# Kernel optimization log

Hardware: AMD Instinct MI355X
Metric: run time of the kernel (lower is better)

The kernel has to match this reference:

```python
import jax, jax.numpy as jnp
import numpy as np

N_SRC = 100000

def setup_inputs() -> dict:
    key = jax.random.key(0)
    k1, k2, k3 = jax.random.split(key, 3)
    feat_src = jax.random.normal(k1, (N_SRC, 64), dtype=jnp.float32)
    edge_src = jax.random.randint(k2, (1250000,), 0, N_SRC, dtype=jnp.int64)
    edge_dst = jax.random.randint(k3, (1250000,), 0, 50000, dtype=jnp.int64)
    return {"feat_src": feat_src, "edge_src": edge_src, "edge_dst": edge_dst, "n_dst": 50000}

def reference(feat_src, edge_src, edge_dst, n_dst):
    n_src = feat_src.shape[0]
    ones = jnp.ones(edge_src.shape[0], dtype=feat_src.dtype)
    # out-degree of src nodes, in-degree of dst nodes
    deg_out = jax.ops.segment_sum(ones, edge_src, num_segments=n_src)
    deg_in = jax.ops.segment_sum(ones, edge_dst, num_segments=n_dst)
    norm_src = jax.lax.rsqrt(jnp.clip(deg_out, 1.0))  # [n_src]
    norm_dst = jax.lax.rsqrt(jnp.clip(deg_in, 1.0))   # [n_dst]
    # gather -> scale -> scatter-sum
    msg = feat_src[edge_src] * norm_src[edge_src][:, None]      # [E, d]
    rst = jax.ops.segment_sum(msg, edge_dst, num_segments=n_dst)  # [n_dst, d]
    return rst * norm_dst[:, None]
```

## Files before the change

### kernel.cpp

```cpp
#include <hip/hip_runtime.h>

#define NFEAT 64
#define SCAN_BLOCKS 128

#define NB_IN  128
#define NB_OUT 64
#define LWORDS 12512

__global__ __launch_bounds__(1024) void v28_hist(
        const int* __restrict__ esrc, const int* __restrict__ edst,
        unsigned char* __restrict__ cnt_in, unsigned char* __restrict__ cnt_out,
        int E, int n_src, int n_dst, int Ec_in, int Ec_out, int srange) {
    __shared__ unsigned int lh[LWORDS];
    int blk = blockIdx.x, t = threadIdx.x, T = blockDim.x;
    const int* idx; unsigned char* row; int rbase, W, lo, hi;
    if (blk < NB_IN) {
        idx = edst; rbase = 0; W = n_dst;
        row = cnt_in + (size_t)blk * n_dst;
        lo = blk * Ec_in; hi = lo + Ec_in;
    } else {
        int p    = (blk - NB_IN) / NB_OUT;
        int brel = (blk - NB_IN) % NB_OUT;
        idx = esrc; rbase = p * srange;
        W = n_src - rbase; if (W > srange) W = srange;
        row = cnt_out + (size_t)brel * n_src + rbase;
        lo = brel * Ec_out; hi = lo + Ec_out;
    }
    if (hi > E) hi = E;
    if (W <= 0) return;
    int Wp = (W + 3) >> 2;
    for (int i = t; i < Wp; i += T) lh[i] = 0;
    __syncthreads();
    if (lo < hi) {
        int nq = (hi - lo) >> 2;
#define V28_H(val)                                                            \
        {                                                                     \
            unsigned r = (unsigned)((val) - rbase);                           \
            if (r < (unsigned)W)                                              \
                atomicAdd(&lh[r >> 2], 1u << ((r & 3) << 3));                 \
        }
        for (int q = t; q < nq; q += T) {
            int i = lo + (q << 2);
            int4 e = *(const int4*)(idx + i);
            V28_H(e.x) V28_H(e.y) V28_H(e.z) V28_H(e.w)
        }
        for (int i = lo + (nq << 2) + t; i < hi; i += T) V28_H(idx[i]);
#undef V28_H
    }
    __syncthreads();
    if ((((uintptr_t)row) & 3) == 0 && (W & 3) == 0) {
        unsigned int* row32 = (unsigned int*)row;
        for (int i = t; i < Wp; i += T) row32[i] = lh[i];
    } else {
        for (int i = t; i < W; i += T)
            row[i] = (unsigned char)((lh[i >> 2] >> ((i & 3) << 3)) & 0xff);
    }
}

__global__ void v28_normscan(const unsigned char* __restrict__ cnt_out,
                             unsigned char* __restrict__ cnt_in,
                             int* __restrict__ deg_in,
                             float* __restrict__ nsrc, float* __restrict__ ndst,
                             int* __restrict__ bsum, int n_src, int n_dst) {
    __shared__ int red[256];
    int b = blockIdx.x, t = threadIdx.x;
    int cs = (n_src + SCAN_BLOCKS - 1) / SCAN_BLOCKS;
    int slo = b * cs, shi = slo + cs; if (shi > n_src) shi = n_src;
    for (int i = slo + t; i < shi; i += 256) {
        const unsigned char* p = cnt_out + i;
        int s = 0;
        for (int j = 0; j < NB_OUT; ++j) { s += *p; p += n_src; }
        nsrc[i] = rsqrtf(fmaxf((float)s, 1.0f));
    }
    int cd = (n_dst + SCAN_BLOCKS - 1) / SCAN_BLOCKS;
    int dlo = b * cd, dhi = dlo + cd; if (dhi > n_dst) dhi = n_dst;
    int tot = 0;
    for (int i = dlo + t; i < dhi; i += 256) {
        unsigned char* p = cnt_in + i;
        int a = 0;
        for (int j = 0; j < NB_IN; ++j) {
            int c = *p;
            *p = (unsigned char)a;
            a += c;
            p += n_dst;
        }
        deg_in[i] = a;
        ndst[i] = rsqrtf(fmaxf((float)a, 1.0f));
        tot += a;
    }
    red[t] = tot;
    __syncthreads();
    for (int o = 128; o > 0; o >>= 1) {
        if (t < o) red[t] += red[t + o];
        __syncthreads();
    }
    if (t == 0) bsum[b] = red[0];
}

__global__ void v28_rowstart(const int* __restrict__ deg_in,
                             const int* __restrict__ bsum,
                             int* __restrict__ row_start, int n_dst) {
    __shared__ int tsum[256];
    __shared__ int boffs;
    int b = blockIdx.x, t = threadIdx.x;
    int cd = (n_dst + SCAN_BLOCKS - 1) / SCAN_BLOCKS;
    int lo = b * cd, hi = lo + cd; if (hi > n_dst) hi = n_dst;
    if (t == 0) {
        int a = 0;
        for (int k = 0; k < b; ++k) a += bsum[k];
        boffs = a;
    }
    int per = (cd + 255) / 256;
    int mylo = lo + t * per;
    int myhi = mylo + per; if (myhi > hi) myhi = hi;
    int s = 0;
    for (int i = mylo; i < myhi; ++i) s += deg_in[i];
    tsum[t] = s;
    __syncthreads();
    if (t == 0) {
        int a = 0;
        for (int k = 0; k < 256; ++k) { int v = tsum[k]; tsum[k] = a; a += v; }
    }
    __syncthreads();
    int a = boffs + tsum[t];
    for (int i = mylo; i < myhi; ++i) { row_start[i] = a; a += deg_in[i]; }
    if (b == SCAN_BLOCKS - 1 && t == 255) row_start[n_dst] = a;
}

__global__ __launch_bounds__(1024) void v28_place(
        const int* __restrict__ esrc, const int* __restrict__ edst,
        const unsigned char* __restrict__ pre, const int* __restrict__ row_start,
        int* __restrict__ sorted_src, int E, int n_dst, int Ec) {
    __shared__ unsigned int lh[LWORDS];
    int b = blockIdx.x, t = threadIdx.x, T = blockDim.x;
    int Wp = (n_dst + 3) >> 2;
    for (int i = t; i < Wp; i += T) lh[i] = 0;
    __syncthreads();
    int lo = b * Ec;
    int hi = lo + Ec; if (hi > E) hi = E;
    if (lo >= hi) return;
    const unsigned char* prow = pre + (size_t)b * n_dst;
    int nq = (hi - lo) >> 2;
#define V28_PL(dd, ss)                                                       \
    {                                                                        \
        unsigned r = (unsigned)(dd);                                         \
        if (r < (unsigned)n_dst) {                                           \
            int sh = (r & 3) << 3;                                           \
            unsigned old = atomicAdd(&lh[r >> 2], 1u << sh);                 \
            int rank = (old >> sh) & 0xff;                                   \
            int slot = row_start[r] + (int)prow[r] + rank;                   \
            if ((unsigned)slot < (unsigned)E) sorted_src[slot] = (ss);       \
        }                                                                    \
    }
    for (int q = t; q < nq; q += T) {
        int i = lo + (q << 2);
        int4 dv = *(const int4*)(edst + i);
        int4 sv = *(const int4*)(esrc + i);
        V28_PL(dv.x, sv.x)
        V28_PL(dv.y, sv.y)
        V28_PL(dv.z, sv.z)
        V28_PL(dv.w, sv.w)
    }
    for (int i = lo + (nq << 2) + t; i < hi; i += T) {
        int d = edst[i];
        int s = esrc[i];
        V28_PL(d, s)
    }
#undef V28_PL
}

__global__ void v26_gather(const float* __restrict__ feat,
                           const int* __restrict__ sorted_src,
                           const int* __restrict__ row_start,
                           const float* __restrict__ nsrc,
                           const float* __restrict__ ndst,
                           float* __restrict__ out,
                           int n_src, int n_dst) {
    int gid = blockIdx.x * blockDim.x + threadIdx.x;
    int d = gid >> 6;
    if (d >= n_dst) return;
    int lane = threadIdx.x & 63;
    int g = lane >> 4;
    int lg = lane & 15;
    int lo = row_start[d], hi = row_start[d + 1];
    int nmax = n_src - 1;
    float4 a0 = {0,0,0,0}, a1 = {0,0,0,0}, a2 = {0,0,0,0}, a3 = {0,0,0,0};
#define V26_G(kk, acc)                                                        \
    {                                                                         \
        int s_ = sorted_src[(kk) + g];                                        \
        s_ = min(max(s_, 0), nmax);                                           \
        float w_ = nsrc[s_];                                                  \
        float4 v_ = *(const float4*)(feat + (size_t)s_ * NFEAT + (lg << 2));  \
        acc.x += v_.x * w_; acc.y += v_.y * w_;                               \
        acc.z += v_.z * w_; acc.w += v_.w * w_;                               \
    }
    int k = lo;
    for (; k + 15 < hi; k += 16) {
        V26_G(k, a0)
        V26_G(k + 4, a1)
        V26_G(k + 8, a2)
        V26_G(k + 12, a3)
    }
    for (; k + 3 < hi; k += 4) {
        V26_G(k, a0)
    }
    if (k + g < hi) {
        V26_G(k, a1)
    }
#undef V26_G
    float4 a;
    a.x = (a0.x + a1.x) + (a2.x + a3.x);
    a.y = (a0.y + a1.y) + (a2.y + a3.y);
    a.z = (a0.z + a1.z) + (a2.z + a3.z);
    a.w = (a0.w + a1.w) + (a2.w + a3.w);
    a.x += __shfl_xor(a.x, 16); a.x += __shfl_xor(a.x, 32);
    a.y += __shfl_xor(a.y, 16); a.y += __shfl_xor(a.y, 32);
    a.z += __shfl_xor(a.z, 16); a.z += __shfl_xor(a.z, 32);
    a.w += __shfl_xor(a.w, 16); a.w += __shfl_xor(a.w, 32);
    if (g == 0) {
        float sc = ndst[d];
        float4 r;
        r.x = a.x * sc; r.y = a.y * sc; r.z = a.z * sc; r.w = a.w * sc;
        *(float4*)(out + (size_t)d * NFEAT + (lg << 2)) = r;
    }
}


__global__ void v23_zero(int* __restrict__ deg_out, int* __restrict__ deg_in,
                         int n_src, int n_dst) {
    int i = blockIdx.x * blockDim.x + threadIdx.x;
    if (i < n_src) deg_out[i] = 0;
    if (i < n_dst) deg_in[i] = 0;
}

__global__ void v23_deg(const int* __restrict__ esrc, const int* __restrict__ edst,
                        int* __restrict__ deg_out, int* __restrict__ deg_in,
                        int E, int n_src, int n_dst) {
    int i = blockIdx.x * blockDim.x + threadIdx.x;
    if (i >= E) return;
    int s = esrc[i];
    int d = edst[i];
    if ((unsigned)s < (unsigned)n_src) atomicAdd(&deg_out[s], 1);
    if ((unsigned)d < (unsigned)n_dst) atomicAdd(&deg_in[d], 1);
}

__global__ void v23_norm(const int* __restrict__ deg_out, const int* __restrict__ deg_in,
                         float* __restrict__ nsrc, float* __restrict__ ndst,
                         int n_src, int n_dst) {
    int i = blockIdx.x * blockDim.x + threadIdx.x;
    if (i < n_src) nsrc[i] = rsqrtf(fmaxf((float)deg_out[i], 1.0f));
    if (i < n_dst) ndst[i] = rsqrtf(fmaxf((float)deg_in[i], 1.0f));
}

__global__ void v23_scan1(const int* __restrict__ deg_in, int* __restrict__ bsum,
                          int n_dst, int chunk) {
    __shared__ int red[256];
    int b = blockIdx.x, t = threadIdx.x;
    int lo = b * chunk;
    int hi = lo + chunk; if (hi > n_dst) hi = n_dst;
    int s = 0;
    for (int i = lo + t; i < hi; i += 256) s += deg_in[i];
    red[t] = s;
    __syncthreads();
    for (int o = 128; o > 0; o >>= 1) {
        if (t < o) red[t] += red[t + o];
        __syncthreads();
    }
    if (t == 0) bsum[b] = red[0];
}

__global__ void v23_scan2(int* __restrict__ bsum, int* __restrict__ boff,
                          int* __restrict__ row_start, int n_dst) {
    if (threadIdx.x == 0) {
        int a = 0;
        for (int k = 0; k < SCAN_BLOCKS; ++k) { boff[k] = a; a += bsum[k]; }
        row_start[n_dst] = a;
    }
}

__global__ void v23_scan3(const int* __restrict__ deg_in, const int* __restrict__ boff,
                          int* __restrict__ row_start, int* __restrict__ cursor,
                          int n_dst, int chunk) {
    __shared__ int tsum[256];
    int b = blockIdx.x, t = threadIdx.x;
    int lo = b * chunk;
    int hi = lo + chunk; if (hi > n_dst) hi = n_dst;
    int per = (chunk + 255) / 256;
    int mylo = lo + t * per;
    int myhi = mylo + per; if (myhi > hi) myhi = hi;
    int s = 0;
    for (int i = mylo; i < myhi; ++i) s += deg_in[i];
    tsum[t] = s;
    __syncthreads();
    if (t == 0) {
        int a = 0;
        for (int k = 0; k < 256; ++k) { int v = tsum[k]; tsum[k] = a; a += v; }
    }
    __syncthreads();
    int a = boff[b] + tsum[t];
    for (int i = mylo; i < myhi; ++i) {
        row_start[i] = a;
        cursor[i] = a;
        a += deg_in[i];
    }
}

__global__ void v23_place(const int* __restrict__ esrc, const int* __restrict__ edst,
                          int* __restrict__ cursor, int* __restrict__ sorted_src,
                          int E, int n_src, int n_dst) {
    int i = blockIdx.x * blockDim.x + threadIdx.x;
    if (i >= E) return;
    int s = esrc[i];
    int d = edst[i];
    if ((unsigned)s >= (unsigned)n_src) return;
    if ((unsigned)d >= (unsigned)n_dst) return;
    int slot = atomicAdd(&cursor[d], 1);
    sorted_src[slot] = s;
}


extern "C" void kernel_launch(void* const* d_in, const int* in_sizes, int n_in,
                              void* d_out, int out_size, void* d_ws, size_t ws_size,
                              hipStream_t stream) {
    const float* feat = (const float*)d_in[0];
    const int* esrc = (const int*)d_in[1];
    const int* edst = (const int*)d_in[2];
    float* out = (float*)d_out;

    const int n_src = in_sizes[0] / NFEAT;
    const int E     = in_sizes[1];
    const int n_dst = out_size / NFEAT;

    const int B = 256;
    int nmax = n_src > n_dst ? n_src : n_dst;
    int chunk = (n_dst + SCAN_BLOCKS - 1) / SCAN_BLOCKS;

    int srange = (((n_src + 1) / 2) + 3) & ~3;

    size_t sz_cnt_in  = ((size_t)NB_IN  * (size_t)n_dst + 255) & ~(size_t)255;
    size_t sz_cnt_out = ((size_t)NB_OUT * (size_t)n_src + 255) & ~(size_t)255;
    size_t sz_fixed = (size_t)E * 4
                    + (size_t)n_dst * 4
                    + (size_t)n_src * 4
                    + (size_t)n_dst * 4
                    + (size_t)(n_dst + 1) * 4
                    + (size_t)n_dst * 4
                    + (size_t)SCAN_BLOCKS * 8 + 512;
    bool big = (ws_size >= sz_cnt_in + sz_cnt_out + sz_fixed)
             && (n_dst <= LWORDS * 4) && (srange <= LWORDS * 4);

    if (big) {
        char* ws = (char*)d_ws;
        size_t off = 0;
        unsigned char* cnt_in  = (unsigned char*)(ws + off); off += sz_cnt_in;
        unsigned char* cnt_out = (unsigned char*)(ws + off); off += sz_cnt_out;
        int*   sorted_src = (int*)(ws + off);   off += (size_t)E * 4;
        int*   deg_in     = (int*)(ws + off);   off += (size_t)n_dst * 4;
        float* nsrc       = (float*)(ws + off); off += (size_t)n_src * 4;
        float* ndst       = (float*)(ws + off); off += (size_t)n_dst * 4;
        int*   row_start  = (int*)(ws + off);   off += (size_t)(n_dst + 1) * 4;
        int*   bsum       = (int*)(ws + off);   off += SCAN_BLOCKS * 4;

        int Ec_in  = (((E + NB_IN  - 1) / NB_IN ) + 3) & ~3;
        int Ec_out = (((E + NB_OUT - 1) / NB_OUT) + 3) & ~3;

        v28_hist<<<NB_IN + 2 * NB_OUT, 1024, 0, stream>>>(
            esrc, edst, cnt_in, cnt_out, E, n_src, n_dst, Ec_in, Ec_out, srange);
        v28_normscan<<<SCAN_BLOCKS, B, 0, stream>>>(
            cnt_out, cnt_in, deg_in, nsrc, ndst, bsum, n_src, n_dst);
        v28_rowstart<<<SCAN_BLOCKS, B, 0, stream>>>(deg_in, bsum, row_start, n_dst);
        v28_place<<<NB_IN, 1024, 0, stream>>>(esrc, edst, cnt_in, row_start,
                                              sorted_src, E, n_dst, Ec_in);
        long long gthreads = (long long)n_dst * 64;
        v26_gather<<<(int)((gthreads + B - 1) / B), B, 0, stream>>>(feat, sorted_src,
                                                                    row_start, nsrc, ndst,
                                                                    out, n_src, n_dst);
    } else {
        char* ws = (char*)d_ws;
        size_t off = 0;
        int*   deg_out    = (int*)(ws + off);   off += (size_t)n_src * 4;
        int*   deg_in     = (int*)(ws + off);   off += (size_t)n_dst * 4;
        float* nsrc       = (float*)(ws + off); off += (size_t)n_src * 4;
        float* ndst       = (float*)(ws + off); off += (size_t)n_dst * 4;
        int*   row_start  = (int*)(ws + off);   off += (size_t)(n_dst + 1) * 4;
        int*   cursor     = (int*)(ws + off);   off += (size_t)n_dst * 4;
        int*   bsum       = (int*)(ws + off);   off += SCAN_BLOCKS * 4;
        int*   boff       = (int*)(ws + off);   off += SCAN_BLOCKS * 4;
        int*   sorted_src = (int*)(ws + off);   off += (size_t)E * 4;

        v23_zero<<<(nmax + B - 1) / B, B, 0, stream>>>(deg_out, deg_in, n_src, n_dst);
        v23_deg<<<(E + B - 1) / B, B, 0, stream>>>(esrc, edst, deg_out, deg_in,
                                                   E, n_src, n_dst);
        v23_norm<<<(nmax + B - 1) / B, B, 0, stream>>>(deg_out, deg_in, nsrc, ndst,
                                                       n_src, n_dst);
        v23_scan1<<<SCAN_BLOCKS, B, 0, stream>>>(deg_in, bsum, n_dst, chunk);
        v23_scan2<<<1, 64, 0, stream>>>(bsum, boff, row_start, n_dst);
        v23_scan3<<<SCAN_BLOCKS, B, 0, stream>>>(deg_in, boff, row_start, cursor,
                                                 n_dst, chunk);
        v23_place<<<(E + B - 1) / B, B, 0, stream>>>(esrc, edst, cursor, sorted_src,
                                                     E, n_src, n_dst);
        long long gthreads = (long long)n_dst * 64;
        v26_gather<<<(int)((gthreads + B - 1) / B), B, 0, stream>>>(feat, sorted_src,
                                                                    row_start, nsrc, ndst,
                                                                    out, n_src, n_dst);
    }
}
```

Measured before the change: 205.4 us.

## Restructure CSR build: 2D-tiled histograms, per-node norm/scan, preloaded place offsets

The fused histogram kernel is split into two launches on 2D grids. Each range tile is sized to fit shared memory, and the block counts rise (256 in, 128 out). The normalisation and scan now run one thread per node, with a single-pass exclusive scan in place of the serial rowstart loop. The place kernel preloads each block's prefix bytes into shared memory so the atomic returns the full rank directly, removing a global byte read per edge. This adds more partial-count rows to reduce and more launches. The fast path now also requires node counts divisible by four and at most 65536 dst nodes.

```diff
diff --git a/kernel.cpp b/kernel.cpp
--- a/kernel.cpp
+++ b/kernel.cpp
@@ -1,39 +1,29 @@
 #include <hip/hip_runtime.h>
 
 #define NFEAT 64
-#define SCAN_BLOCKS 128
-
-#define NB_IN  128
-#define NB_OUT 64
-#define LWORDS 12512
-
-__global__ __launch_bounds__(1024) void v28_hist(
-        const int* __restrict__ esrc, const int* __restrict__ edst,
-        unsigned char* __restrict__ cnt_in, unsigned char* __restrict__ cnt_out,
-        int E, int n_src, int n_dst, int Ec_in, int Ec_out, int srange) {
-    __shared__ unsigned int lh[LWORDS];
-    int blk = blockIdx.x, t = threadIdx.x, T = blockDim.x;
-    const int* idx; unsigned char* row; int rbase, W, lo, hi;
-    if (blk < NB_IN) {
-        idx = edst; rbase = 0; W = n_dst;
-        row = cnt_in + (size_t)blk * n_dst;
-        lo = blk * Ec_in; hi = lo + Ec_in;
-    } else {
-        int p    = (blk - NB_IN) / NB_OUT;
-        int brel = (blk - NB_IN) % NB_OUT;
-        idx = esrc; rbase = p * srange;
-        W = n_src - rbase; if (W > srange) W = srange;
-        row = cnt_out + (size_t)brel * n_src + rbase;
-        lo = brel * Ec_out; hi = lo + Ec_out;
-    }
-    if (hi > E) hi = E;
+
+#define PR8 50048
+#define PW8 (PR8 / 4)
+#define NB_IN  256
+#define NB_OUT 128
+
+__global__ __launch_bounds__(1024) void v32_hist(
+        const int* __restrict__ idx, unsigned char* __restrict__ cnt,
+        int E, int n, int Ec) {
+    __shared__ unsigned int lh[PW8];
+    int b = blockIdx.x, t = threadIdx.x, T = blockDim.x;
+    int rbase = blockIdx.y * PR8;
+    int rend = rbase + PR8; if (rend > n) rend = n;
+    int W = rend - rbase;
     if (W <= 0) return;
     int Wp = (W + 3) >> 2;
     for (int i = t; i < Wp; i += T) lh[i] = 0;
     __syncthreads();
+    int lo = b * Ec;
+    int hi = lo + Ec; if (hi > E) hi = E;
     if (lo < hi) {
         int nq = (hi - lo) >> 2;
-#define V28_H(val)                                                            \
+#define V32_H(val)                                                            \
         {                                                                     \
             unsigned r = (unsigned)((val) - rbase);                           \
             if (r < (unsigned)W)                                              \
@@ -42,13 +32,14 @@
         for (int q = t; q < nq; q += T) {
             int i = lo + (q << 2);
             int4 e = *(const int4*)(idx + i);
-            V28_H(e.x) V28_H(e.y) V28_H(e.z) V28_H(e.w)
+            V32_H(e.x) V32_H(e.y) V32_H(e.z) V32_H(e.w)
         }
-        for (int i = lo + (nq << 2) + t; i < hi; i += T) V28_H(idx[i]);
-#undef V28_H
-    }
-    __syncthreads();
-    if ((((uintptr_t)row) & 3) == 0 && (W & 3) == 0) {
+        for (int i = lo + (nq << 2) + t; i < hi; i += T) V32_H(idx[i]);
+#undef V32_H
+    }
+    __syncthreads();
+    unsigned char* row = cnt + (size_t)b * n + rbase;
+    if (((((uintptr_t)row) & 3) == 0) && ((W & 3) == 0)) {
         unsigned int* row32 = (unsigned int*)row;
         for (int i = t; i < Wp; i += T) row32[i] = lh[i];
     } else {
@@ -57,27 +48,27 @@
     }
 }
 
-__global__ void v28_normscan(const unsigned char* __restrict__ cnt_out,
-                             unsigned char* __restrict__ cnt_in,
-                             int* __restrict__ deg_in,
-                             float* __restrict__ nsrc, float* __restrict__ ndst,
-                             int* __restrict__ bsum, int n_src, int n_dst) {
+__global__ __launch_bounds__(256) void v32_norm(
+        const unsigned char* __restrict__ cnt_out,
+        unsigned char* __restrict__ cnt_in,
+        int* __restrict__ deg_in,
+        float* __restrict__ nsrc, float* __restrict__ ndst,
+        int* __restrict__ bsum, int n_src, int n_dst) {
     __shared__ int red[256];
     int b = blockIdx.x, t = threadIdx.x;
-    int cs = (n_src + SCAN_BLOCKS - 1) / SCAN_BLOCKS;
-    int slo = b * cs, shi = slo + cs; if (shi > n_src) shi = n_src;
-    for (int i = slo + t; i < shi; i += 256) {
+    int i = b * 256 + t;
+    if (i < n_src) {
         const unsigned char* p = cnt_out + i;
         int s = 0;
+#pragma unroll 8
         for (int j = 0; j < NB_OUT; ++j) { s += *p; p += n_src; }
         nsrc[i] = rsqrtf(fmaxf((float)s, 1.0f));
     }
-    int cd = (n_dst + SCAN_BLOCKS - 1) / SCAN_BLOCKS;
-    int dlo = b * cd, dhi = dlo + cd; if (dhi > n_dst) dhi = n_dst;
-    int tot = 0;
-    for (int i = dlo + t; i < dhi; i += 256) {
+    int dval = 0;
+    if (i < n_dst) {
         unsigned char* p = cnt_in + i;
         int a = 0;
+#pragma unroll 8
         for (int j = 0; j < NB_IN; ++j) {
             int c = *p;
             *p = (unsigned char)a;
@@ -86,87 +77,109 @@
         }
         deg_in[i] = a;
         ndst[i] = rsqrtf(fmaxf((float)a, 1.0f));
-        tot += a;
-    }
-    red[t] = tot;
-    __syncthreads();
-    for (int o = 128; o > 0; o >>= 1) {
-        if (t < o) red[t] += red[t + o];
-        __syncthreads();
-    }
-    if (t == 0) bsum[b] = red[0];
-}
-
-__global__ void v28_rowstart(const int* __restrict__ deg_in,
-                             const int* __restrict__ bsum,
-                             int* __restrict__ row_start, int n_dst) {
+        dval = a;
+    }
+    int nch = (n_dst + 255) >> 8;
+    if (b < nch) {
+        red[t] = dval;
+        __syncthreads();
+        for (int o = 128; o > 0; o >>= 1) {
+            if (t < o) red[t] += red[t + o];
+            __syncthreads();
+        }
+        if (t == 0) bsum[b] = red[0];
+    }
+}
+
+__global__ __launch_bounds__(256) void v32_scan23(
+        const int* __restrict__ deg_in, const int* __restrict__ bsum,
+        int* __restrict__ row_start, int n_dst) {
+    __shared__ int bs[256];
     __shared__ int tsum[256];
-    __shared__ int boffs;
     int b = blockIdx.x, t = threadIdx.x;
-    int cd = (n_dst + SCAN_BLOCKS - 1) / SCAN_BLOCKS;
-    int lo = b * cd, hi = lo + cd; if (hi > n_dst) hi = n_dst;
-    if (t == 0) {
-        int a = 0;
-        for (int k = 0; k < b; ++k) a += bsum[k];
-        boffs = a;
-    }
-    int per = (cd + 255) / 256;
-    int mylo = lo + t * per;
-    int myhi = mylo + per; if (myhi > hi) myhi = hi;
-    int s = 0;
-    for (int i = mylo; i < myhi; ++i) s += deg_in[i];
-    tsum[t] = s;
-    __syncthreads();
-    if (t == 0) {
-        int a = 0;
-        for (int k = 0; k < 256; ++k) { int v = tsum[k]; tsum[k] = a; a += v; }
-    }
-    __syncthreads();
-    int a = boffs + tsum[t];
-    for (int i = mylo; i < myhi; ++i) { row_start[i] = a; a += deg_in[i]; }
-    if (b == SCAN_BLOCKS - 1 && t == 255) row_start[n_dst] = a;
-}
-
-__global__ __launch_bounds__(1024) void v28_place(
+    int nch = (n_dst + 255) >> 8;
+    bs[t] = (t < nch) ? bsum[t] : 0;
+    __syncthreads();
+    for (int off = 1; off < 256; off <<= 1) {
+        int v = (t >= off) ? bs[t - off] : 0;
+        __syncthreads();
+        bs[t] += v;
+        __syncthreads();
+    }
+    int i = b * 256 + t;
+    int dval = (i < n_dst) ? deg_in[i] : 0;
+    tsum[t] = dval;
+    __syncthreads();
+    for (int off = 1; off < 256; off <<= 1) {
+        int v = (t >= off) ? tsum[t - off] : 0;
+        __syncthreads();
+        tsum[t] += v;
+        __syncthreads();
+    }
+    int boffs = b ? bs[b - 1] : 0;
+    if (i < n_dst) row_start[i] = boffs + tsum[t] - dval;
+    if (b == 0 && t == 0) row_start[n_dst] = bs[nch - 1];
+}
+
+__global__ __launch_bounds__(1024) void v32_place(
         const int* __restrict__ esrc, const int* __restrict__ edst,
         const unsigned char* __restrict__ pre, const int* __restrict__ row_start,
         int* __restrict__ sorted_src, int E, int n_dst, int Ec) {
-    __shared__ unsigned int lh[LWORDS];
+    __shared__ unsigned int lh[PW8];
     int b = blockIdx.x, t = threadIdx.x, T = blockDim.x;
-    int Wp = (n_dst + 3) >> 2;
-    for (int i = t; i < Wp; i += T) lh[i] = 0;
+    int rbase = blockIdx.y * PR8;
+    int rend = rbase + PR8; if (rend > n_dst) rend = n_dst;
+    int W = rend - rbase;
+    if (W <= 0) return;
+    const unsigned char* prow = pre + (size_t)b * n_dst + rbase;
+    int full = W >> 2;
+    if ((((uintptr_t)prow) & 3) == 0) {
+        const unsigned int* prow32 = (const unsigned int*)prow;
+        for (int i = t; i < full; i += T) lh[i] = prow32[i];
+        if (t == 0) {
+            for (int r = full << 2; r < W; ++r) {
+                int sh = (r & 3) << 3;
+                unsigned w = lh[r >> 2] & ~(0xffu << sh);
+                lh[r >> 2] = w | ((unsigned)prow[r] << sh);
+            }
+        }
+    } else {
+        for (int i = t; i < ((W + 3) >> 2); i += T) lh[i] = 0;
+        __syncthreads();
+        for (int r = t; r < W; r += T)
+            atomicOr(&lh[r >> 2], (unsigned)prow[r] << ((r & 3) << 3));
+    }
     __syncthreads();
     int lo = b * Ec;
     int hi = lo + Ec; if (hi > E) hi = E;
     if (lo >= hi) return;
-    const unsigned char* prow = pre + (size_t)b * n_dst;
     int nq = (hi - lo) >> 2;
-#define V28_PL(dd, ss)                                                       \
-    {                                                                        \
-        unsigned r = (unsigned)(dd);                                         \
-        if (r < (unsigned)n_dst) {                                           \
-            int sh = (r & 3) << 3;                                           \
-            unsigned old = atomicAdd(&lh[r >> 2], 1u << sh);                 \
-            int rank = (old >> sh) & 0xff;                                   \
-            int slot = row_start[r] + (int)prow[r] + rank;                   \
-            if ((unsigned)slot < (unsigned)E) sorted_src[slot] = (ss);       \
-        }                                                                    \
+#define V32_PL(dd, ss)                                                        \
+    {                                                                         \
+        unsigned r = (unsigned)((dd) - rbase);                                \
+        if (r < (unsigned)W) {                                                \
+            int sh = (r & 3) << 3;                                            \
+            unsigned old = atomicAdd(&lh[r >> 2], 1u << sh);                  \
+            int pr = (int)((old >> sh) & 0xff);                               \
+            int slot = row_start[dd] + pr;                                    \
+            if ((unsigned)slot < (unsigned)E) sorted_src[slot] = (ss);        \
+        }                                                                     \
     }
     for (int q = t; q < nq; q += T) {
         int i = lo + (q << 2);
         int4 dv = *(const int4*)(edst + i);
         int4 sv = *(const int4*)(esrc + i);
-        V28_PL(dv.x, sv.x)
-        V28_PL(dv.y, sv.y)
-        V28_PL(dv.z, sv.z)
-        V28_PL(dv.w, sv.w)
+        V32_PL(dv.x, sv.x)
+        V32_PL(dv.y, sv.y)
+        V32_PL(dv.z, sv.z)
+        V32_PL(dv.w, sv.w)
     }
     for (int i = lo + (nq << 2) + t; i < hi; i += T) {
         int d = edst[i];
         int s = esrc[i];
-        V28_PL(d, s)
-    }
-#undef V28_PL
+        V32_PL(d, s)
+    }
+#undef V32_PL
 }
 
 __global__ void v26_gather(const float* __restrict__ feat,
@@ -225,6 +238,7 @@
     }
 }
 
+#define SCAN_BLOCKS 128
 
 __global__ void v23_zero(int* __restrict__ deg_out, int* __restrict__ deg_in,
                          int n_src, int n_dst) {
@@ -232,7 +246,6 @@
     if (i < n_src) deg_out[i] = 0;
     if (i < n_dst) deg_in[i] = 0;
 }
-
 __global__ void v23_deg(const int* __restrict__ esrc, const int* __restrict__ edst,
                         int* __restrict__ deg_out, int* __restrict__ deg_in,
                         int E, int n_src, int n_dst) {
@@ -243,7 +256,6 @@
     if ((unsigned)s < (unsigned)n_src) atomicAdd(&deg_out[s], 1);
     if ((unsigned)d < (unsigned)n_dst) atomicAdd(&deg_in[d], 1);
 }
-
 __global__ void v23_norm(const int* __restrict__ deg_out, const int* __restrict__ deg_in,
                          float* __restrict__ nsrc, float* __restrict__ ndst,
                          int n_src, int n_dst) {
@@ -251,7 +263,6 @@
     if (i < n_src) nsrc[i] = rsqrtf(fmaxf((float)deg_out[i], 1.0f));
     if (i < n_dst) ndst[i] = rsqrtf(fmaxf((float)deg_in[i], 1.0f));
 }
-
 __global__ void v23_scan1(const int* __restrict__ deg_in, int* __restrict__ bsum,
                           int n_dst, int chunk) {
     __shared__ int red[256];
@@ -268,7 +279,6 @@
     }
     if (t == 0) bsum[b] = red[0];
 }
-
 __global__ void v23_scan2(int* __restrict__ bsum, int* __restrict__ boff,
                           int* __restrict__ row_start, int n_dst) {
     if (threadIdx.x == 0) {
@@ -277,7 +287,6 @@
         row_start[n_dst] = a;
     }
 }
-
 __global__ void v23_scan3(const int* __restrict__ deg_in, const int* __restrict__ boff,
                           int* __restrict__ row_start, int* __restrict__ cursor,
                           int n_dst, int chunk) {
@@ -304,7 +313,6 @@
         a += deg_in[i];
     }
 }
-
 __global__ void v23_place(const int* __restrict__ esrc, const int* __restrict__ edst,
                           int* __restrict__ cursor, int* __restrict__ sorted_src,
                           int E, int n_src, int n_dst) {
@@ -335,19 +343,18 @@
     int nmax = n_src > n_dst ? n_src : n_dst;
     int chunk = (n_dst + SCAN_BLOCKS - 1) / SCAN_BLOCKS;
 
-    int srange = (((n_src + 1) / 2) + 3) & ~3;
-
     size_t sz_cnt_in  = ((size_t)NB_IN  * (size_t)n_dst + 255) & ~(size_t)255;
     size_t sz_cnt_out = ((size_t)NB_OUT * (size_t)n_src + 255) & ~(size_t)255;
     size_t sz_fixed = (size_t)E * 4
                     + (size_t)n_dst * 4
                     + (size_t)n_src * 4
                     + (size_t)n_dst * 4
+                    + (size_t)n_dst * 4
                     + (size_t)(n_dst + 1) * 4
-                    + (size_t)n_dst * 4
-                    + (size_t)SCAN_BLOCKS * 8 + 512;
+                    + 256 * 4 + SCAN_BLOCKS * 4 + 512;
+    int nch = (n_dst + 255) >> 8;
     bool big = (ws_size >= sz_cnt_in + sz_cnt_out + sz_fixed)
-             && (n_dst <= LWORDS * 4) && (srange <= LWORDS * 4);
+             && (nch <= 256) && ((n_dst & 3) == 0) && ((n_src & 3) == 0);
 
     if (big) {
         char* ws = (char*)d_ws;
@@ -358,19 +365,26 @@
         int*   deg_in     = (int*)(ws + off);   off += (size_t)n_dst * 4;
         float* nsrc       = (float*)(ws + off); off += (size_t)n_src * 4;
         float* ndst       = (float*)(ws + off); off += (size_t)n_dst * 4;
+        int*   cursor     = (int*)(ws + off);   off += (size_t)n_dst * 4;
         int*   row_start  = (int*)(ws + off);   off += (size_t)(n_dst + 1) * 4;
-        int*   bsum       = (int*)(ws + off);   off += SCAN_BLOCKS * 4;
+        int*   bsum       = (int*)(ws + off);   off += 256 * 4;
+        (void)cursor;
 
         int Ec_in  = (((E + NB_IN  - 1) / NB_IN ) + 3) & ~3;
         int Ec_out = (((E + NB_OUT - 1) / NB_OUT) + 3) & ~3;
-
-        v28_hist<<<NB_IN + 2 * NB_OUT, 1024, 0, stream>>>(
-            esrc, edst, cnt_in, cnt_out, E, n_src, n_dst, Ec_in, Ec_out, srange);
-        v28_normscan<<<SCAN_BLOCKS, B, 0, stream>>>(
-            cnt_out, cnt_in, deg_in, nsrc, ndst, bsum, n_src, n_dst);
-        v28_rowstart<<<SCAN_BLOCKS, B, 0, stream>>>(deg_in, bsum, row_start, n_dst);
-        v28_place<<<NB_IN, 1024, 0, stream>>>(esrc, edst, cnt_in, row_start,
-                                              sorted_src, E, n_dst, Ec_in);
+        int P_in  = (n_dst + PR8 - 1) / PR8;
+        int P_out = (n_src + PR8 - 1) / PR8;
+
+        dim3 gout(NB_OUT, P_out), gin(NB_IN, P_in);
+
+        v32_hist<<<gout, 1024, 0, stream>>>(esrc, cnt_out, E, n_src, Ec_out);
+        v32_hist<<<gin,  1024, 0, stream>>>(edst, cnt_in,  E, n_dst, Ec_in);
+        v32_norm<<<(nmax + B - 1) / B, B, 0, stream>>>(cnt_out, cnt_in, deg_in,
+                                                       nsrc, ndst, bsum,
+                                                       n_src, n_dst);
+        v32_scan23<<<nch, B, 0, stream>>>(deg_in, bsum, row_start, n_dst);
+        v32_place<<<gin, 1024, 0, stream>>>(esrc, edst, cnt_in, row_start,
+                                            sorted_src, E, n_dst, Ec_in);
         long long gthreads = (long long)n_dst * 64;
         v26_gather<<<(int)((gthreads + B - 1) / B), B, 0, stream>>>(feat, sorted_src,
                                                                     row_start, nsrc, ndst,
```

Result: faster. 197.0 us (-4.1%).
